# Performance work log

Hardware: AMD Instinct MI355X
Metric: run time of the kernel (lower is better)

## Reference

```python
import jax, jax.numpy as jnp
import numpy as np

D_MODEL = 1024
N_HEADS = 16
HEAD_DIM = D_MODEL // N_HEADS


def setup_inputs() -> dict:
    key = jax.random.key(0)
    ks = jax.random.split(key, 9)
    B, T = 4, 2048
    s = 1.0 / np.sqrt(D_MODEL)
    inp = {
        'x': jax.random.normal(ks[0], (B, T, D_MODEL), jnp.float32),
        'W_q': jax.random.normal(ks[1], (D_MODEL, D_MODEL), jnp.float32) * s,
        'b_q': jnp.zeros((D_MODEL,), jnp.float32),
        'W_k': jax.random.normal(ks[2], (D_MODEL, D_MODEL), jnp.float32) * s,
        'b_k': jnp.zeros((D_MODEL,), jnp.float32),
        'W_v': jax.random.normal(ks[3], (D_MODEL, D_MODEL), jnp.float32) * s,
        'b_v': jnp.zeros((D_MODEL,), jnp.float32),
        'W_o': jax.random.normal(ks[4], (D_MODEL, D_MODEL), jnp.float32) * s,
        'b_o': jnp.zeros((D_MODEL,), jnp.float32),
    }
    return inp


def reference(x, W_q, b_q, W_k, b_k, W_v, b_v, W_o, b_o):
    B, T, _ = x.shape
    # torch Linear: y = x @ W.T + b
    def proj(W, b):
        y = jnp.einsum('btd,ed->bte', x, W) + b
        return y.reshape(B, T, N_HEADS, HEAD_DIM).transpose(0, 2, 1, 3)  # (B,H,T,hd)
    Q = proj(W_q, b_q)
    K = proj(W_k, b_k)
    V = proj(W_v, b_v)
    scores = jnp.einsum('bhqd,bhkd->bhqk', Q, K) / np.sqrt(HEAD_DIM)
    causal = jnp.tril(jnp.ones((T, T), bool))
    scores = jnp.where(causal[None, None, :, :], scores, -jnp.inf)
    attn = jax.nn.softmax(scores, axis=-1)  # dropout = identity (eval)
    out = jnp.einsum('bhqk,bhkd->bhqd', attn, V)
    out = out.transpose(0, 2, 1, 3).reshape(B, T, D_MODEL)
    return jnp.einsum('btd,ed->bte', out, W_o) + b_o
```

## Files before the change

kernel.cpp:

```cpp
#include <hip/hip_runtime.h>
#include <hip/hip_bf16.h>

#define D_MODEL 1024
#define T_SEQ   2048
#define BATCH   4
#define NHEADS  16
#define HDIM    64
#define M_ROWS  (BATCH * T_SEQ)
#define QSCALE  (0.125f * 1.44269504088896340736f)

typedef unsigned short ushortT;
typedef __attribute__((ext_vector_type(4))) float f32x4;
typedef __attribute__((ext_vector_type(8))) short s16x8;

#define GP(p) ((const __attribute__((address_space(1))) void*)(p))
#define LP(p) ((__attribute__((address_space(3))) void*)(p))

static __device__ __forceinline__ ushortT f2b(float f) {
    union { float f; unsigned u; } v; v.f = f;
    unsigned r = v.u + 0x7fffu + ((v.u >> 16) & 1u);
    return (ushortT)(r >> 16);
}

static __device__ __forceinline__ unsigned cvtpk(float lo, float hi) {
    unsigned r;
    asm("v_cvt_pk_bf16_f32 %0, %1, %2" : "=v"(r) : "v"(lo), "v"(hi));
    return r;
}

__global__ void cast_all(const float* __restrict__ x,
                         const float* __restrict__ Wq, const float* __restrict__ Wk,
                         const float* __restrict__ Wv, const float* __restrict__ Wo,
                         ushortT* __restrict__ dst) {
    const int i = blockIdx.x * 256 + threadIdx.x;
    const float* src; int g, ob;
    if (i < 1048576)      { src = x;  g = i;           ob = 0; }
    else if (i < 1179648) { src = Wq; g = i - 1048576; ob = 1048576; }
    else if (i < 1310720) { src = Wk; g = i - 1179648; ob = 1179648; }
    else if (i < 1441792) { src = Wv; g = i - 1310720; ob = 1310720; }
    else                  { src = Wo; g = i - 1441792; ob = 1441792; }
    const float4* s = (const float4*)src;
    float4 a = s[g * 2], b = s[g * 2 + 1];
    s16x8 r;
    r[0] = f2b(a.x); r[1] = f2b(a.y); r[2] = f2b(a.z); r[3] = f2b(a.w);
    r[4] = f2b(b.x); r[5] = f2b(b.y); r[6] = f2b(b.z); r[7] = f2b(b.w);
    ((s16x8*)dst)[ob + (g ^ ((g >> 7) & 7))] = r;
}


#define GEMM_PREAMBLE()                                                  \
    const int tid  = threadIdx.x;                                        \
    const int wave = tid >> 6, lane = tid & 63;                          \
    const int wm = wave >> 1, wn = wave & 1;                             \
    const int lr = lane & 15, lh = lane >> 4;                            \
    const int srow = tid >> 3;                                           \
    const int sg   = tid & 7;                                            \
    f32x4 acc[4][4] = {};                                                \
    const ushortT* Ag = A  + (size_t)(m0 + srow) * 1024 + sg * 8;        \
    const ushortT* Bg = Bw + (size_t)(n0 + srow) * 1024 + sg * 8;

#define STAGE_G(k0)                                                                    \
    do {                                                                               \
        _Pragma("unroll")                                                              \
        for (int is = 0; is < 4; ++is) {                                               \
            __builtin_amdgcn_global_load_lds(GP(Ag + (size_t)(is * 32) * 1024 + (k0)), \
                                             LP(&As[is * 2048 + tid * 8]), 16, 0, 0);  \
            __builtin_amdgcn_global_load_lds(GP(Bg + (size_t)(is * 32) * 1024 + (k0)), \
                                             LP(&Bs[is * 2048 + tid * 8]), 16, 0, 0);  \
        }                                                                              \
    } while (0)

#define COMPUTE_G()                                                                    \
    do {                                                                               \
        _Pragma("unroll")                                                              \
        for (int kk = 0; kk < 2; ++kk) {                                               \
            s16x8 af[4], bfr[4];                                                       \
            const int g = ((kk * 4 + lh) ^ (lr & 7)) * 8;                              \
            _Pragma("unroll")                                                          \
            for (int i = 0; i < 4; ++i)                                                \
                af[i] = *(const s16x8*)&As[(wm * 64 + i * 16 + lr) * 64 + g];          \
            _Pragma("unroll")                                                          \
            for (int j = 0; j < 4; ++j)                                                \
                bfr[j] = *(const s16x8*)&Bs[(wn * 64 + j * 16 + lr) * 64 + g];         \
            __builtin_amdgcn_s_setprio(1);                                             \
            _Pragma("unroll")                                                          \
            for (int i = 0; i < 4; ++i)                                                \
                _Pragma("unroll")                                                      \
                for (int j = 0; j < 4; ++j)                                            \
                    acc[i][j] = __builtin_amdgcn_mfma_f32_16x16x32_bf16(af[i], bfr[j], acc[i][j], 0, 0, 0); \
            __builtin_amdgcn_s_setprio(0);                                             \
        }                                                                              \
    } while (0)

#define GEMM_KLOOP()                        \
    for (int t = 0; t < 16; ++t) {          \
        STAGE_G(t * 64);                    \
        __syncthreads();                    \
        COMPUTE_G();                        \
        __syncthreads();                    \
    }

__global__ __launch_bounds__(256, 5) void qkv_gemm(
    const ushortT* __restrict__ A,
    const ushortT* __restrict__ Wq, const ushortT* __restrict__ Wk, const ushortT* __restrict__ Wv,
    const float* __restrict__ bq, const float* __restrict__ bk, const float* __restrict__ bv,
    ushortT* __restrict__ Qb, ushortT* __restrict__ Kb, ushortT* __restrict__ Vtb)
{
    __shared__ __attribute__((aligned(16))) ushortT As[128 * 64];
    __shared__ __attribute__((aligned(16))) ushortT Bs[128 * 64];

    const int seg = blockIdx.y >> 3;
    const int m0 = blockIdx.x * 128, n0 = (blockIdx.y & 7) * 128;
    const ushortT* Bw   = (seg == 0) ? Wq : (seg == 1) ? Wk : Wv;
    const float*   bias = (seg == 0) ? bq : (seg == 1) ? bk : bv;
    const float    scale = (seg == 0) ? QSCALE : 1.0f;

    GEMM_PREAMBLE();
    GEMM_KLOOP();

    ushortT* outp = (seg == 0) ? Qb : (seg == 1) ? Kb : Vtb;
    #pragma unroll
    for (int i = 0; i < 4; ++i) {
        #pragma unroll
        for (int j = 0; j < 4; ++j) {
            const int c = n0 + wn * 64 + j * 16 + lr;
            const float bv_ = bias[c];
            #pragma unroll
            for (int e = 0; e < 4; ++e) {
                const int r = m0 + wm * 64 + i * 16 + lh * 4 + e;
                const float val = (acc[i][j][e] + bv_) * scale;
                const int b = r >> 11, t = r & 2047;
                const int h = c >> 6,  d = c & 63;
                size_t idx;
                if (seg == 2)      idx = ((size_t)(b * NHEADS + h) * HDIM + d) * T_SEQ + (t ^ ((d & 7) << 3));
                else if (seg == 1) idx = ((size_t)(b * NHEADS + h) * T_SEQ + t) * HDIM + (d ^ ((t & 7) << 3));
                else               idx = ((size_t)(b * NHEADS + h) * T_SEQ + t) * HDIM + d;
                outp[idx] = f2b(val);
            }
        }
    }
}

__global__ __launch_bounds__(256, 5) void out_gemm(
    const ushortT* __restrict__ A, const ushortT* __restrict__ Bw,
    const float* __restrict__ bias, float* __restrict__ outp)
{
    __shared__ __attribute__((aligned(16))) ushortT As[128 * 64];
    __shared__ __attribute__((aligned(16))) ushortT Bs[128 * 64];

    const int m0 = blockIdx.x * 128, n0 = blockIdx.y * 128;

    GEMM_PREAMBLE();
    GEMM_KLOOP();

    #pragma unroll
    for (int i = 0; i < 4; ++i) {
        #pragma unroll
        for (int j = 0; j < 4; ++j) {
            const int c = n0 + wn * 64 + j * 16 + lr;
            const float bv_ = bias[c];
            #pragma unroll
            for (int e = 0; e < 4; ++e) {
                const int r = m0 + wm * 64 + i * 16 + lh * 4 + e;
                outp[(size_t)r * 1024 + c] = acc[i][j][e] + bv_;
            }
        }
    }
}

__global__ __launch_bounds__(512, 6) void attn_fwd(
    const ushortT* __restrict__ Qb, const ushortT* __restrict__ Kb,
    const ushortT* __restrict__ Vt, ushortT* __restrict__ Ob)
{
    __shared__ __attribute__((aligned(16))) ushortT Ks[2][64 * 64];
    __shared__ __attribute__((aligned(16))) ushortT Vs[2][64 * 64];
    __shared__ __attribute__((aligned(16))) ushortT Ps[8][16 * 64];

    const int tid = threadIdx.x;
    const int w = tid >> 6, lane = tid & 63;
    const int lr = lane & 15, lh = lane >> 4;

    const int blk  = blockIdx.x;
    const int bh   = (blk & 7) * 8 + ((blk >> 3) & 7);
    const int grp  = blk >> 6;
    const int qg64 = (15 - grp) * 2;
    const int q0   = qg64 * 64;
    const int last = qg64 + 1;

    const int srow = tid >> 3;
    const int sk   = (tid & 7) * 8;

    const ushortT* Kbh = Kb + (size_t)bh * T_SEQ * HDIM;
    const ushortT* Vbh = Vt + (size_t)bh * HDIM * T_SEQ;
    const int b = bh >> 4, h = bh & 15;

    const int g0 = (lh       ^ (lr & 7)) * 8;
    const int g1 = ((4 + lh) ^ (lr & 7)) * 8;

    #define STAGE(buf, kt_) do { \
        const int k0_ = (kt_) * 64; \
        __builtin_amdgcn_global_load_lds(GP(Kbh + (size_t)(k0_ + srow) * HDIM + sk), \
                                         LP(&Ks[buf][srow * 64 + sk]), 16, 0, 0); \
        __builtin_amdgcn_global_load_lds(GP(Vbh + (size_t)srow * T_SEQ + k0_ + sk), \
                                         LP(&Vs[buf][srow * 64 + sk]), 16, 0, 0); \
    } while (0)

    STAGE(0, 0);

    const ushortT* qrow = Qb + ((size_t)bh * T_SEQ + q0 + w * 16 + lr) * HDIM;
    const s16x8 qf0 = *(const s16x8*)(qrow + lh * 8);
    const s16x8 qf1 = *(const s16x8*)(qrow + 32 + lh * 8);

    float m_r = -1e30f, l_r = 0.f;
    f32x4 o[4] = {};

    const int dt = qg64 + (w >> 2);

    __syncthreads();

    for (int kt = 0; kt <= last; ++kt) {
        const int cur = kt & 1;
        if (kt < last) STAGE(cur ^ 1, kt + 1);

        if (kt <= dt) {
            f32x4 s[4];
            __builtin_amdgcn_s_setprio(1);
            #pragma unroll
            for (int ni = 0; ni < 4; ++ni) {
                const int rr = ni * 16 + lr;
                s16x8 b0 = *(const s16x8*)&Ks[cur][rr * 64 + g0];
                s16x8 b1 = *(const s16x8*)&Ks[cur][rr * 64 + g1];
                f32x4 t = {};
                t = __builtin_amdgcn_mfma_f32_16x16x32_bf16(b0, qf0, t, 0, 0, 0);
                t = __builtin_amdgcn_mfma_f32_16x16x32_bf16(b1, qf1, t, 0, 0, 0);
                s[ni] = t;
            }
            __builtin_amdgcn_s_setprio(0);

            if (kt == dt) {
                #pragma unroll
                for (int ni = 0; ni < 4; ++ni)
                    #pragma unroll
                    for (int e = 0; e < 4; ++e)
                        if (ni * 16 + lh * 4 + e > (w & 3) * 16 + lr) s[ni][e] = -1e30f;
            }

            float pm;
            {
                float a0 = fmaxf(fmaxf(s[0][0], s[0][1]), fmaxf(s[0][2], s[0][3]));
                float a1 = fmaxf(fmaxf(s[1][0], s[1][1]), fmaxf(s[1][2], s[1][3]));
                float a2 = fmaxf(fmaxf(s[2][0], s[2][1]), fmaxf(s[2][2], s[2][3]));
                float a3 = fmaxf(fmaxf(s[3][0], s[3][1]), fmaxf(s[3][2], s[3][3]));
                pm = fmaxf(fmaxf(a0, a1), fmaxf(a2, a3));
            }
            pm = fmaxf(pm, __shfl_xor(pm, 16, 64));
            pm = fmaxf(pm, __shfl_xor(pm, 32, 64));

            if (!__all(pm - m_r <= 8.f)) {
                const float mn = fmaxf(m_r, pm);
                const float sc = exp2f(m_r - mn);
                l_r *= sc;
                #pragma unroll
                for (int ni = 0; ni < 4; ++ni) o[ni] *= sc;
                m_r = mn;
            }

            float rs = 0.f;
            #pragma unroll
            for (int ni = 0; ni < 4; ++ni)
                #pragma unroll
                for (int e = 0; e < 4; ++e) {
                    const float pv_ = exp2f(s[ni][e] - m_r);
                    s[ni][e] = pv_;
                    rs += pv_;
                }
            rs += __shfl_xor(rs, 16, 64);
            rs += __shfl_xor(rs, 32, 64);
            l_r += rs;

            #pragma unroll
            for (int ni = 0; ni < 4; ++ni) {
                const unsigned u0 = cvtpk(s[ni][0], s[ni][1]);
                const unsigned u1 = cvtpk(s[ni][2], s[ni][3]);
                *(uint2*)&Ps[w][lr * 64 + ((ni * 16 + lh * 4) ^ ((lr & 7) << 3))] = make_uint2(u0, u1);
            }
            __asm__ volatile("s_waitcnt lgkmcnt(0)" ::: "memory");
            __builtin_amdgcn_sched_barrier(0);
            const s16x8 pf0 = *(const s16x8*)&Ps[w][lr * 64 + g0];
            const s16x8 pf1 = *(const s16x8*)&Ps[w][lr * 64 + g1];

            __builtin_amdgcn_s_setprio(1);
            #pragma unroll
            for (int ni = 0; ni < 4; ++ni) {
                const int dd = ni * 16 + lr;
                s16x8 v0 = *(const s16x8*)&Vs[cur][dd * 64 + g0];
                s16x8 v1 = *(const s16x8*)&Vs[cur][dd * 64 + g1];
                o[ni] = __builtin_amdgcn_mfma_f32_16x16x32_bf16(v0, pf0, o[ni], 0, 0, 0);
                o[ni] = __builtin_amdgcn_mfma_f32_16x16x32_bf16(v1, pf1, o[ni], 0, 0, 0);
            }
            __builtin_amdgcn_s_setprio(0);
        }
        __syncthreads();
    }

    const int t = q0 + w * 16 + lr;
    const float inv = 1.f / l_r;
    const size_t base = ((size_t)(b * T_SEQ) + t) * D_MODEL;
    #pragma unroll
    for (int ni = 0; ni < 4; ++ni) {
        const unsigned u0 = cvtpk(o[ni][0] * inv, o[ni][1] * inv);
        const unsigned u1 = cvtpk(o[ni][2] * inv, o[ni][3] * inv);
        const int c = h * HDIM + ni * 16 + lh * 4;
        *(uint2*)&Ob[base + (c ^ ((t & 7) << 3))] = make_uint2(u0, u1);
    }
}

extern "C" void kernel_launch(void* const* d_in, const int* in_sizes, int n_in,
                              void* d_out, int out_size, void* d_ws, size_t ws_size,
                              hipStream_t stream) {
    const float* x  = (const float*)d_in[0];
    const float* Wq = (const float*)d_in[1];
    const float* bq = (const float*)d_in[2];
    const float* Wk = (const float*)d_in[3];
    const float* bk = (const float*)d_in[4];
    const float* Wv = (const float*)d_in[5];
    const float* bv = (const float*)d_in[6];
    const float* Wo = (const float*)d_in[7];
    const float* bo = (const float*)d_in[8];

    ushortT* xb  = (ushortT*)d_ws;
    ushortT* Wqb = xb  + (size_t)M_ROWS * D_MODEL;
    ushortT* Wkb = Wqb + (size_t)D_MODEL * D_MODEL;
    ushortT* Wvb = Wkb + (size_t)D_MODEL * D_MODEL;
    ushortT* Wob = Wvb + (size_t)D_MODEL * D_MODEL;
    ushortT* Qb  = Wob + (size_t)D_MODEL * D_MODEL;
    ushortT* Kb  = Qb  + (size_t)M_ROWS * D_MODEL;
    ushortT* Vtb = Kb  + (size_t)M_ROWS * D_MODEL;
    ushortT* Ob  = Vtb + (size_t)M_ROWS * D_MODEL;

    cast_all<<<6144, 256, 0, stream>>>(x, Wq, Wk, Wv, Wo, xb);

    qkv_gemm<<<dim3(64, 24), 256, 0, stream>>>(xb, Wqb, Wkb, Wvb, bq, bk, bv, Qb, Kb, Vtb);

    attn_fwd<<<1024, 512, 0, stream>>>(Qb, Kb, Vtb, Ob);

    out_gemm<<<dim3(64, 8), 256, 0, stream>>>(Ob, Wob, bo, (float*)d_out);
}
```

Measured before the change: 309.5 us.

## Rewrite projection GEMMs as 256x256 tiles with double-buffered LDS pipeline

```diff
diff --git a/kernel.cpp b/kernel.cpp
--- a/kernel.cpp
+++ b/kernel.cpp
@@ -48,121 +48,152 @@
 }
 
 
-#define GEMM_PREAMBLE()                                                  \
+#define G256_PRE()                                                       \
     const int tid  = threadIdx.x;                                        \
     const int wave = tid >> 6, lane = tid & 63;                          \
-    const int wm = wave >> 1, wn = wave & 1;                             \
+    const int wm = wave >> 2, wn = wave & 3;                             \
     const int lr = lane & 15, lh = lane >> 4;                            \
-    const int srow = tid >> 3;                                           \
-    const int sg   = tid & 7;                                            \
-    f32x4 acc[4][4] = {};                                                \
-    const ushortT* Ag = A  + (size_t)(m0 + srow) * 1024 + sg * 8;        \
-    const ushortT* Bg = Bw + (size_t)(n0 + srow) * 1024 + sg * 8;
-
-#define STAGE_G(k0)                                                                    \
-    do {                                                                               \
-        _Pragma("unroll")                                                              \
-        for (int is = 0; is < 4; ++is) {                                               \
-            __builtin_amdgcn_global_load_lds(GP(Ag + (size_t)(is * 32) * 1024 + (k0)), \
-                                             LP(&As[is * 2048 + tid * 8]), 16, 0, 0);  \
-            __builtin_amdgcn_global_load_lds(GP(Bg + (size_t)(is * 32) * 1024 + (k0)), \
-                                             LP(&Bs[is * 2048 + tid * 8]), 16, 0, 0);  \
-        }                                                                              \
+    const int srow = tid >> 3, sg = tid & 7;                             \
+    const int gA0 = (lh ^ (lr & 7)) * 8;                                 \
+    const int gA1 = ((4 + lh) ^ (lr & 7)) * 8;                           \
+    f32x4 acc[8][4] = {};                                                \
+    const ushortT* Ag = A  + (size_t)(m0  + srow) * 1024 + sg * 8;       \
+    const ushortT* Bg = Bw + (size_t)(n0s + srow) * 1024 + sg * 8;
+
+#define STG(buf, kt)                                                                     \
+    do {                                                                                 \
+        const int k0_ = (kt) * 64;                                                       \
+        _Pragma("unroll")                                                                \
+        for (int is = 0; is < 4; ++is) {                                                 \
+            __builtin_amdgcn_global_load_lds(GP(Ag + (size_t)(is * 64) * 1024 + k0_),    \
+                                             LP(&As[buf][is * 4096 + tid * 8]), 16, 0, 0); \
+            __builtin_amdgcn_global_load_lds(GP(Bg + (size_t)(is * 64) * 1024 + k0_),    \
+                                             LP(&Bs[buf][is * 4096 + tid * 8]), 16, 0, 0); \
+        }                                                                                \
     } while (0)
 
-#define COMPUTE_G()                                                                    \
-    do {                                                                               \
-        _Pragma("unroll")                                                              \
-        for (int kk = 0; kk < 2; ++kk) {                                               \
-            s16x8 af[4], bfr[4];                                                       \
-            const int g = ((kk * 4 + lh) ^ (lr & 7)) * 8;                              \
-            _Pragma("unroll")                                                          \
-            for (int i = 0; i < 4; ++i)                                                \
-                af[i] = *(const s16x8*)&As[(wm * 64 + i * 16 + lr) * 64 + g];          \
-            _Pragma("unroll")                                                          \
-            for (int j = 0; j < 4; ++j)                                                \
-                bfr[j] = *(const s16x8*)&Bs[(wn * 64 + j * 16 + lr) * 64 + g];         \
-            __builtin_amdgcn_s_setprio(1);                                             \
-            _Pragma("unroll")                                                          \
-            for (int i = 0; i < 4; ++i)                                                \
-                _Pragma("unroll")                                                      \
-                for (int j = 0; j < 4; ++j)                                            \
-                    acc[i][j] = __builtin_amdgcn_mfma_f32_16x16x32_bf16(af[i], bfr[j], acc[i][j], 0, 0, 0); \
-            __builtin_amdgcn_s_setprio(0);                                             \
-        }                                                                              \
-    } while (0)
-
-#define GEMM_KLOOP()                        \
-    for (int t = 0; t < 16; ++t) {          \
-        STAGE_G(t * 64);                    \
-        __syncthreads();                    \
-        COMPUTE_G();                        \
-        __syncthreads();                    \
-    }
-
-__global__ __launch_bounds__(256, 5) void qkv_gemm(
+#define RD_A(mh)                                                         \
+    { _Pragma("unroll")                                                  \
+      for (int mi = 0; mi < 4; ++mi) {                                   \
+          const int rb = (wm * 128 + (mh) * 64 + mi * 16 + lr) * 64;     \
+          af[mi][0] = *(const s16x8*)&As[cur][rb + gA0];                 \
+          af[mi][1] = *(const s16x8*)&As[cur][rb + gA1];                 \
+      } }
+
+#define RD_B(nh)                                                         \
+    { _Pragma("unroll")                                                  \
+      for (int ni = 0; ni < 2; ++ni) {                                   \
+          const int rb = (wn * 64 + (nh) * 32 + ni * 16 + lr) * 64;      \
+          bf_[ni][0] = *(const s16x8*)&Bs[cur][rb + gA0];                 \
+          bf_[ni][1] = *(const s16x8*)&Bs[cur][rb + gA1];                 \
+      } }
+
+#define MM(mh, nh)                                                                       \
+    { __builtin_amdgcn_s_setprio(1);                                                     \
+      _Pragma("unroll")                                                                  \
+      for (int mi = 0; mi < 4; ++mi)                                                     \
+          _Pragma("unroll")                                                              \
+          for (int ni = 0; ni < 2; ++ni) {                                               \
+              acc[(mh)*4+mi][(nh)*2+ni] = __builtin_amdgcn_mfma_f32_16x16x32_bf16(       \
+                  af[mi][0], bf_[ni][0], acc[(mh)*4+mi][(nh)*2+ni], 0, 0, 0);            \
+              acc[(mh)*4+mi][(nh)*2+ni] = __builtin_amdgcn_mfma_f32_16x16x32_bf16(       \
+                  af[mi][1], bf_[ni][1], acc[(mh)*4+mi][(nh)*2+ni], 0, 0, 0);            \
+          }                                                                              \
+      __builtin_amdgcn_s_setprio(0); }
+
+#define LGKM0 do { asm volatile("s_waitcnt lgkmcnt(0)" ::: "memory"); \
+                   __builtin_amdgcn_sched_barrier(0); } while (0)
+
+#define G256_KLOOP()                                                     \
+    STG(0, 0);                                                           \
+    STG(1, 1);                                                           \
+    _Pragma("unroll 1")                                                  \
+    for (int t = 0; t < 16; ++t) {                                       \
+        const int cur = t & 1;                                           \
+        if (t < 15) { asm volatile("s_waitcnt vmcnt(8)" ::: "memory"); } \
+        else        { asm volatile("s_waitcnt vmcnt(0)" ::: "memory"); } \
+        __builtin_amdgcn_s_barrier();                                    \
+        __builtin_amdgcn_sched_barrier(0);                               \
+        s16x8 af[4][2], bf_[2][2];                                       \
+        RD_A(0); RD_B(0); LGKM0; MM(0, 0);                               \
+        RD_B(1); LGKM0; MM(0, 1);                                        \
+        RD_A(1); LGKM0; MM(1, 1);                                        \
+        RD_B(0); LGKM0;                                                  \
+        __builtin_amdgcn_s_barrier();                                    \
+        __builtin_amdgcn_sched_barrier(0);                               \
+        if (t < 14) STG(cur, t + 2);                                     \
+        MM(1, 0);                                                        \
+    }
+
+__global__ __launch_bounds__(512, 2) void qkv_gemm(
     const ushortT* __restrict__ A,
     const ushortT* __restrict__ Wq, const ushortT* __restrict__ Wk, const ushortT* __restrict__ Wv,
     const float* __restrict__ bq, const float* __restrict__ bk, const float* __restrict__ bv,
     ushortT* __restrict__ Qb, ushortT* __restrict__ Kb, ushortT* __restrict__ Vtb)
 {
-    __shared__ __attribute__((aligned(16))) ushortT As[128 * 64];
-    __shared__ __attribute__((aligned(16))) ushortT Bs[128 * 64];
-
-    const int seg = blockIdx.y >> 3;
-    const int m0 = blockIdx.x * 128, n0 = (blockIdx.y & 7) * 128;
+    __shared__ __attribute__((aligned(16))) ushortT As[2][256 * 64];
+    __shared__ __attribute__((aligned(16))) ushortT Bs[2][256 * 64];
+
+    const int swz = (blockIdx.x & 7) * 48 + (blockIdx.x >> 3);
+    const int m0  = (swz / 12) * 256;
+    const int y   = swz % 12;
+    const int seg = y >> 2;
+    const int n0s = (y & 3) * 256;
+
     const ushortT* Bw   = (seg == 0) ? Wq : (seg == 1) ? Wk : Wv;
     const float*   bias = (seg == 0) ? bq : (seg == 1) ? bk : bv;
     const float    scale = (seg == 0) ? QSCALE : 1.0f;
-
-    GEMM_PREAMBLE();
-    GEMM_KLOOP();
-
-    ushortT* outp = (seg == 0) ? Qb : (seg == 1) ? Kb : Vtb;
+    ushortT*       outp = (seg == 0) ? Qb : (seg == 1) ? Kb : Vtb;
+
+    G256_PRE();
+    G256_KLOOP();
+
     #pragma unroll
-    for (int i = 0; i < 4; ++i) {
+    for (int mi = 0; mi < 8; ++mi) {
         #pragma unroll
-        for (int j = 0; j < 4; ++j) {
-            const int c = n0 + wn * 64 + j * 16 + lr;
+        for (int na = 0; na < 4; ++na) {
+            const int c = n0s + wn * 64 + na * 16 + lr;
             const float bv_ = bias[c];
             #pragma unroll
             for (int e = 0; e < 4; ++e) {
-                const int r = m0 + wm * 64 + i * 16 + lh * 4 + e;
-                const float val = (acc[i][j][e] + bv_) * scale;
-                const int b = r >> 11, t = r & 2047;
+                const int r = m0 + wm * 128 + mi * 16 + lh * 4 + e;
+                const float val = (acc[mi][na][e] + bv_) * scale;
+                const int bb = r >> 11, tt = r & 2047;
                 const int h = c >> 6,  d = c & 63;
                 size_t idx;
-                if (seg == 2)      idx = ((size_t)(b * NHEADS + h) * HDIM + d) * T_SEQ + (t ^ ((d & 7) << 3));
-                else if (seg == 1) idx = ((size_t)(b * NHEADS + h) * T_SEQ + t) * HDIM + (d ^ ((t & 7) << 3));
-                else               idx = ((size_t)(b * NHEADS + h) * T_SEQ + t) * HDIM + d;
+                if (seg == 2)      idx = ((size_t)(bb * NHEADS + h) * HDIM + d) * T_SEQ + (tt ^ ((d & 7) << 3));
+                else if (seg == 1) idx = ((size_t)(bb * NHEADS + h) * T_SEQ + tt) * HDIM + (d ^ ((tt & 7) << 3));
+                else               idx = ((size_t)(bb * NHEADS + h) * T_SEQ + tt) * HDIM + d;
                 outp[idx] = f2b(val);
             }
         }
     }
 }
 
-__global__ __launch_bounds__(256, 5) void out_gemm(
+__global__ __launch_bounds__(512, 2) void out_gemm(
     const ushortT* __restrict__ A, const ushortT* __restrict__ Bw,
     const float* __restrict__ bias, float* __restrict__ outp)
 {
-    __shared__ __attribute__((aligned(16))) ushortT As[128 * 64];
-    __shared__ __attribute__((aligned(16))) ushortT Bs[128 * 64];
-
-    const int m0 = blockIdx.x * 128, n0 = blockIdx.y * 128;
-
-    GEMM_PREAMBLE();
-    GEMM_KLOOP();
+    __shared__ __attribute__((aligned(16))) ushortT As[2][256 * 64];
+    __shared__ __attribute__((aligned(16))) ushortT Bs[2][256 * 64];
+
+    const int swz = (blockIdx.x & 7) * 16 + (blockIdx.x >> 3);
+    const int m0  = (swz / 4) * 256;
+    const int n0s = (swz % 4) * 256;
+
+    G256_PRE();
+    G256_KLOOP();
 
     #pragma unroll
-    for (int i = 0; i < 4; ++i) {
+    for (int mi = 0; mi < 8; ++mi) {
         #pragma unroll
-        for (int j = 0; j < 4; ++j) {
-            const int c = n0 + wn * 64 + j * 16 + lr;
+        for (int na = 0; na < 4; ++na) {
+            const int c = n0s + wn * 64 + na * 16 + lr;
             const float bv_ = bias[c];
             #pragma unroll
             for (int e = 0; e < 4; ++e) {
-                const int r = m0 + wm * 64 + i * 16 + lh * 4 + e;
-                outp[(size_t)r * 1024 + c] = acc[i][j][e] + bv_;
+                const int r = m0 + wm * 128 + mi * 16 + lh * 4 + e;
+                outp[(size_t)r * 1024 + c] = acc[mi][na][e] + bv_;
             }
         }
     }
@@ -340,9 +371,9 @@
 
     cast_all<<<6144, 256, 0, stream>>>(x, Wq, Wk, Wv, Wo, xb);
 
-    qkv_gemm<<<dim3(64, 24), 256, 0, stream>>>(xb, Wqb, Wkb, Wvb, bq, bk, bv, Qb, Kb, Vtb);
+    qkv_gemm<<<384, 512, 0, stream>>>(xb, Wqb, Wkb, Wvb, bq, bk, bv, Qb, Kb, Vtb);
 
     attn_fwd<<<1024, 512, 0, stream>>>(Qb, Kb, Vtb, Ob);
 
-    out_gemm<<<dim3(64, 8), 256, 0, stream>>>(Ob, Wob, bo, (float*)d_out);
-}
+    out_gemm<<<128, 512, 0, stream>>>(Ob, Wob, bo, (float*)d_out);
+}
```

After: 290.5 us. -6.2%, faster.
